# Kernel optimization log

Hardware: AMD Instinct MI355X
Metric: run time of the kernel (lower is better)

## Reference

```python
import jax, jax.numpy as jnp
import numpy as np

NUM_HEADS = 16
R_MIN = 16
R_MAX = 64


def setup_inputs() -> dict:
    key = jax.random.key(0)
    ks = jax.random.split(key, 12)
    bs, S, H = 4, 2048, 1024
    hidden_states = jax.random.normal(ks[0], (bs, S, H), dtype=jnp.float32)
    # Linear layers: y = x @ W.T + b (torch convention, W is [out, in])
    wscale = 1.0 / np.sqrt(H)
    Wq = jax.random.normal(ks[1], (H, H), dtype=jnp.float32) * wscale
    bq = jnp.zeros((H,), dtype=jnp.float32)
    Wk = jax.random.normal(ks[2], (H, H), dtype=jnp.float32) * wscale
    bk = jnp.zeros((H,), dtype=jnp.float32)
    Wv = jax.random.normal(ks[3], (H, H), dtype=jnp.float32) * wscale
    bv = jnp.zeros((H,), dtype=jnp.float32)
    Wo = jax.random.normal(ks[4], (H, H), dtype=jnp.float32) * wscale
    bo = jnp.zeros((H,), dtype=jnp.float32)
    # xavier_uniform for proj_k/proj_v over last two dims (seq_len, r_max)
    xs = float(np.sqrt(6.0 / (S + R_MAX)))
    proj_k = jax.random.uniform(ks[5], (NUM_HEADS, S, R_MAX), dtype=jnp.float32, minval=-xs, maxval=xs)
    proj_v = jax.random.uniform(ks[6], (NUM_HEADS, S, R_MAX), dtype=jnp.float32, minval=-xs, maxval=xs)
    return {
        'hidden_states': hidden_states,
        'Wq': Wq, 'bq': bq, 'Wk': Wk, 'bk': bk, 'Wv': Wv, 'bv': bv,
        'Wo': Wo, 'bo': bo, 'proj_k': proj_k, 'proj_v': proj_v,
    }


def reference(hidden_states, Wq, bq, Wk, bk, Wv, bv, Wo, bo, proj_k, proj_v):
    bs, S, H = hidden_states.shape
    nh = NUM_HEADS
    hd = H // nh

    def heads(x):  # [b,s,H] -> [b,h,s,d]
        return x.reshape(bs, S, nh, hd).transpose(0, 2, 1, 3)

    q = heads(hidden_states @ Wq.T + bq)
    k = heads(hidden_states @ Wk.T + bk)
    v = heads(hidden_states @ Wv.T + bv)

    # dynamic rank from per-sample variance (torch .var is unbiased -> ddof=1)
    batch_var = jnp.var(hidden_states.reshape(bs, -1), axis=1, ddof=1)
    var_norm = (batch_var - batch_var.min()) / (batch_var.max() - batch_var.min() + 1e-6)
    curr_r = jnp.round(R_MIN + var_norm.mean() * (R_MAX - R_MIN)).astype(jnp.int32)

    # low-rank projection of K/V along sequence; compute full r_max, mask at softmax
    key_proj = jnp.einsum('bhld,hlk->bhkd', k, proj_k)      # [b,h,R,d]
    value_proj = jnp.einsum('bhld,hlk->bhkd', v, proj_v)    # [b,h,R,d]

    scores = jnp.einsum('bhsd,bhkd->bhsk', q, key_proj) / jnp.sqrt(jnp.float32(hd))
    rank_mask = jnp.arange(R_MAX) < curr_r                  # [R]
    scores = jnp.where(rank_mask, scores, -jnp.inf)
    attn_probs = jax.nn.softmax(scores, axis=-1)            # zeros beyond curr_r
    # dropout is identity in eval mode
    context = jnp.einsum('bhsk,bhkd->bhsd', attn_probs, value_proj)
    context = context.transpose(0, 2, 1, 3).reshape(bs, S, H)
    output = context @ Wo.T + bo
    return output, attn_probs, curr_r
```

## Files before the change

kernel.cpp:

```cpp
#include <hip/hip_runtime.h>


typedef unsigned short u16;
typedef short s16x8 __attribute__((ext_vector_type(8)));
typedef unsigned short u16x8 __attribute__((ext_vector_type(8)));
typedef float f32x4 __attribute__((ext_vector_type(4)));

#define GLL16(gp, lp) __builtin_amdgcn_global_load_lds( \
    (const __attribute__((address_space(1))) void*)(gp), \
    (__attribute__((address_space(3))) void*)(lp), 16, 0, 0)

__device__ __forceinline__ u16 f2bf(float f) {
    unsigned u = __float_as_uint(f);
    u += 0x7fffu + ((u >> 16) & 1u);
    return (u16)(u >> 16);
}

__device__ __forceinline__ f32x4 mfma16(s16x8 a, s16x8 b, f32x4 c) {
    return __builtin_amdgcn_mfma_f32_16x16x32_bf16(a, b, c, 0, 0, 0);
}

__global__ __launch_bounds__(256) void cast_hs_var_k(const float* __restrict__ hs,
        u16* __restrict__ out, double* __restrict__ red) {
    int t = threadIdx.x;
    size_t base = (size_t)blockIdx.x * 8192;
    double s = 0.0, s2 = 0.0;
    #pragma unroll
    for (int i = 0; i < 4; ++i) {
        size_t idx = base + (size_t)i * 2048 + (size_t)t * 8;
        float4 a = *(const float4*)(hs + idx);
        float4 c = *(const float4*)(hs + idx + 4);
        s  += (double)a.x + (double)a.y + (double)a.z + (double)a.w
            + (double)c.x + (double)c.y + (double)c.z + (double)c.w;
        s2 += (double)a.x * a.x + (double)a.y * a.y + (double)a.z * a.z + (double)a.w * a.w
            + (double)c.x * c.x + (double)c.y * c.y + (double)c.z * c.z + (double)c.w * c.w;
        u16x8 o;
        o[0] = f2bf(a.x); o[1] = f2bf(a.y); o[2] = f2bf(a.z); o[3] = f2bf(a.w);
        o[4] = f2bf(c.x); o[5] = f2bf(c.y); o[6] = f2bf(c.z); o[7] = f2bf(c.w);
        *(u16x8*)(out + idx) = o;
    }
    __shared__ double sa[256], sb[256];
    sa[t] = s; sb[t] = s2;
    __syncthreads();
    for (int o = 128; o > 0; o >>= 1) {
        if (t < o) { sa[t] += sa[t + o]; sb[t] += sb[t + o]; }
        __syncthreads();
    }
    if (t == 0) { red[blockIdx.x * 2] = sa[0]; red[blockIdx.x * 2 + 1] = sb[0]; }
}

__global__ __launch_bounds__(256) void compute_r_k(const double* __restrict__ red,
        int* __restrict__ currp, float* __restrict__ outr) {
    int t = threadIdx.x, lane = t & 63, b = t >> 6;
    double s = 0.0, s2 = 0.0;
    #pragma unroll
    for (int j = 0; j < 4; ++j) {
        int idx = b * 256 + j * 64 + lane;
        s += red[idx * 2]; s2 += red[idx * 2 + 1];
    }
    #pragma unroll
    for (int o = 1; o < 64; o <<= 1) { s += __shfl_xor(s, o); s2 += __shfl_xor(s2, o); }
    __shared__ double vs[4];
    if (lane == 0) {
        const double N = 2097152.0;
        vs[b] = (s2 - s * s / N) / (N - 1.0);
    }
    __syncthreads();
    if (t == 0) {
        double mn = vs[0], mx = vs[0];
        for (int i = 1; i < 4; ++i) { mn = fmin(mn, vs[i]); mx = fmax(mx, vs[i]); }
        double mean = 0.0;
        for (int i = 0; i < 4; ++i) mean += (vs[i] - mn) / (mx - mn + 1e-6);
        mean *= 0.25;
        double r = rint(16.0 + mean * 48.0);
        *currp = (int)r;
        *outr = (float)r;
    }
}

__global__ __launch_bounds__(256) void prep_k(const float* __restrict__ w0,
        const float* __restrict__ w1, const float* __restrict__ w2,
        const float* __restrict__ w3, u16* __restrict__ wout,
        const float* __restrict__ p0, const float* __restrict__ p1,
        u16* __restrict__ q0, u16* __restrict__ q1,
        const float* __restrict__ bq, const float* __restrict__ bk,
        const float* __restrict__ bv, float* __restrict__ biascat) {
    __shared__ float tl[64][65];
    int bid = blockIdx.x, t = threadIdx.x;
    if (bid < 2048) {
        int mat = bid >> 9;
        int off = ((bid & 511) * 256 + t) * 8;
        const float* src = (mat == 0) ? w0 : (mat == 1) ? w1 : (mat == 2) ? w2 : w3;
        float4 a = *(const float4*)(src + off);
        float4 c = *(const float4*)(src + off + 4);
        u16x8 o;
        o[0] = f2bf(a.x); o[1] = f2bf(a.y); o[2] = f2bf(a.z); o[3] = f2bf(a.w);
        o[4] = f2bf(c.x); o[5] = f2bf(c.y); o[6] = f2bf(c.z); o[7] = f2bf(c.w);
        *(u16x8*)(wout + (size_t)mat * 1048576 + off) = o;
    } else if (bid < 3072) {
        int bid2 = bid - 2048;
        int which = bid2 >> 9, bi = bid2 & 511;
        const float* p = which ? p1 : p0;
        u16* pt = which ? q1 : q0;
        int h = bi >> 5, lb = bi & 31;
        {
            int l = t >> 2, r0 = (t & 3) * 16;
            const float* src = p + ((size_t)(h * 2048 + lb * 64 + l)) * 64 + r0;
            #pragma unroll
            for (int u = 0; u < 4; ++u) {
                float4 v = *(const float4*)(src + u * 4);
                tl[l][r0 + u * 4 + 0] = v.x; tl[l][r0 + u * 4 + 1] = v.y;
                tl[l][r0 + u * 4 + 2] = v.z; tl[l][r0 + u * 4 + 3] = v.w;
            }
        }
        __syncthreads();
        {
            int r = t >> 2, l0 = (t & 3) * 16;
            u16x8 o0, o1;
            #pragma unroll
            for (int j = 0; j < 8; ++j) { o0[j] = f2bf(tl[l0 + j][r]); o1[j] = f2bf(tl[l0 + 8 + j][r]); }
            u16* dst = pt + ((size_t)(h * 64 + r)) * 2048 + lb * 64 + l0;
            *(u16x8*)dst = o0;
            *(u16x8*)(dst + 8) = o1;
        }
    } else {
        for (int i = t; i < 3072; i += 256) {
            float v = (i < 1024) ? bq[i] : (i < 2048) ? bk[i - 1024] : bv[i - 2048];
            biascat[i] = v;
        }
    }
}

__global__ __launch_bounds__(512, 2) void qkv_gemm_k(const u16* __restrict__ Ag,
        const u16* __restrict__ Wcat, const float* __restrict__ biascat,
        u16* __restrict__ C) {
    __shared__ u16 lds[40960];
    int bid = blockIdx.x;
    int swz = (bid & 7) * 32 + (bid >> 3);
    int bm = swz >> 3, bn = swz & 7;
    int t = threadIdx.x, lane = t & 63, w = t >> 6, wr = w >> 2, wc = w & 3;

    int srow = w * 16 + (lane >> 2);
    int slog = (((lane & 3) ^ ((lane >> 3) & 3)) << 3);
    const u16* asrc0 = Ag + (size_t)(bm * 256 + srow) * 1024 + slog;
    const u16* bsrc0 = Wcat + (size_t)(bn * 384 + srow) * 1024 + slog;

#define STAGEA(kts, h) GLL16(asrc0 + (h) * 131072 + (kts) * 32, \
                             &lds[(((kts) & 1) * 8192) + (h) * 4096 + w * 512])
#define STAGEB(kts, h) GLL16(bsrc0 + (h) * 131072 + (kts) * 32, \
                             &lds[16384 + (((kts) & 1) * 12288) + (h) * 4096 + w * 512])

    int pcol = (((lane >> 4) ^ (((lane & 15) >> 1) & 3)) << 3);
    int arow0 = (wr * 128 + (lane & 15)) * 32 + pcol;
    int brow0 = 16384 + (wc * 96 + (lane & 15)) * 32 + pcol;

    f32x4 zero4 = {0.f, 0.f, 0.f, 0.f};
    f32x4 acc[8][6];
    #pragma unroll
    for (int m = 0; m < 8; ++m)
        #pragma unroll
        for (int n = 0; n < 6; ++n) acc[m][n] = zero4;

    STAGEA(0, 0); STAGEA(0, 1); STAGEB(0, 0); STAGEB(0, 1); STAGEB(0, 2);
    STAGEA(1, 0); STAGEA(1, 1);
    asm volatile("s_waitcnt vmcnt(2)" ::: "memory");
    __builtin_amdgcn_s_barrier();
    asm volatile("" ::: "memory");

    for (int kt = 0; kt < 32; ++kt) {
        int abase = (kt & 1) * 8192 + arow0;
        int bbase = (kt & 1) * 12288 + brow0;
        s16x8 af[8], bf0, bf1;

        #pragma unroll
        for (int m = 0; m < 8; ++m) af[m] = *(const s16x8*)&lds[abase + m * 512];
        bf0 = *(const s16x8*)&lds[bbase];
        bf1 = *(const s16x8*)&lds[bbase + 512];
        if (kt < 31) { STAGEB(kt + 1, 0); STAGEB(kt + 1, 1); }
        asm volatile("s_waitcnt lgkmcnt(0)" ::: "memory");
        __builtin_amdgcn_s_barrier();
        __builtin_amdgcn_s_setprio(1);
        #pragma unroll
        for (int m = 0; m < 8; ++m) {
            acc[m][0] = mfma16(af[m], bf0, acc[m][0]);
            acc[m][1] = mfma16(af[m], bf1, acc[m][1]);
        }
        __builtin_amdgcn_s_setprio(0);
        __builtin_amdgcn_s_barrier();
        asm volatile("" ::: "memory");

        bf0 = *(const s16x8*)&lds[bbase + 1024];
        bf1 = *(const s16x8*)&lds[bbase + 1536];
        if (kt < 31) STAGEB(kt + 1, 2);
        if (kt < 30) STAGEA(kt + 2, 0);
        asm volatile("s_waitcnt lgkmcnt(0)" ::: "memory");
        __builtin_amdgcn_s_barrier();
        __builtin_amdgcn_s_setprio(1);
        #pragma unroll
        for (int m = 0; m < 8; ++m) {
            acc[m][2] = mfma16(af[m], bf0, acc[m][2]);
            acc[m][3] = mfma16(af[m], bf1, acc[m][3]);
        }
        __builtin_amdgcn_s_setprio(0);
        __builtin_amdgcn_s_barrier();
        asm volatile("" ::: "memory");

        bf0 = *(const s16x8*)&lds[bbase + 2048];
        bf1 = *(const s16x8*)&lds[bbase + 2560];
        if (kt < 30) STAGEA(kt + 2, 1);
        if (kt < 30) { asm volatile("s_waitcnt vmcnt(2)" ::: "memory"); }
        else if (kt == 30) { asm volatile("s_waitcnt vmcnt(0)" ::: "memory"); }
        asm volatile("s_waitcnt lgkmcnt(0)" ::: "memory");
        __builtin_amdgcn_s_barrier();
        __builtin_amdgcn_s_setprio(1);
        #pragma unroll
        for (int m = 0; m < 8; ++m) {
            acc[m][4] = mfma16(af[m], bf0, acc[m][4]);
            acc[m][5] = mfma16(af[m], bf1, acc[m][5]);
        }
        __builtin_amdgcn_s_setprio(0);
        __builtin_amdgcn_s_barrier();
        asm volatile("" ::: "memory");
    }

    float bias[6];
    #pragma unroll
    for (int n = 0; n < 6; ++n)
        bias[n] = biascat[bn * 384 + wc * 96 + n * 16 + (lane & 15)];
    #pragma unroll
    for (int m = 0; m < 8; ++m) {
        int row0 = bm * 256 + wr * 128 + m * 16 + ((lane >> 4) << 2);
        #pragma unroll
        for (int n = 0; n < 6; ++n) {
            int col = bn * 384 + wc * 96 + n * 16 + (lane & 15);
            #pragma unroll
            for (int v = 0; v < 4; ++v)
                C[(size_t)(row0 + v) * 3072 + col] = f2bf(acc[m][n][v] + bias[n]);
        }
    }
#undef STAGEA
#undef STAGEB
}

__global__ __launch_bounds__(256) void gemm_bt_k(const u16* __restrict__ Ag,
        const u16* __restrict__ Bg, const float* __restrict__ biasg,
        float* __restrict__ Cg) {
    __shared__ u16 at[2][4096];
    __shared__ u16 bt[2][4096];
    int bm = blockIdx.x, bn = blockIdx.y;
    int t = threadIdx.x, lane = t & 63, w = t >> 6, wr = w >> 1, wc = w & 1;
    const u16* ag = Ag + (size_t)(bm * 128 + w * 32 + (lane >> 2)) * 1024 + (lane & 3) * 8;
    const u16* bg = Bg + (size_t)(bn * 128 + w * 32 + (lane >> 2)) * 1024 + (lane & 3) * 8;

    f32x4 zero4 = {0.f, 0.f, 0.f, 0.f};
    f32x4 acc[4][4];
    #pragma unroll
    for (int i = 0; i < 4; ++i)
        #pragma unroll
        for (int j = 0; j < 4; ++j) acc[i][j] = zero4;

    GLL16(ag,         &at[0][w * 1024]);
    GLL16(ag + 16384, &at[0][w * 1024 + 512]);
    GLL16(bg,         &bt[0][w * 1024]);
    GLL16(bg + 16384, &bt[0][w * 1024 + 512]);
    __syncthreads();

    int cur = 0;
    for (int kk = 0; kk < 32; ++kk) {
        if (kk < 31) {
            const u16* an = ag + (kk + 1) * 32;
            const u16* bn2 = bg + (kk + 1) * 32;
            GLL16(an,          &at[cur ^ 1][w * 1024]);
            GLL16(an + 16384,  &at[cur ^ 1][w * 1024 + 512]);
            GLL16(bn2,         &bt[cur ^ 1][w * 1024]);
            GLL16(bn2 + 16384, &bt[cur ^ 1][w * 1024 + 512]);
        }
        s16x8 af[4], bf[4];
        #pragma unroll
        for (int i = 0; i < 4; ++i)
            af[i] = *(const s16x8*)&at[cur][(wr * 64 + i * 16 + (lane & 15)) * 32 + (lane >> 4) * 8];
        #pragma unroll
        for (int j = 0; j < 4; ++j)
            bf[j] = *(const s16x8*)&bt[cur][(wc * 64 + j * 16 + (lane & 15)) * 32 + (lane >> 4) * 8];
        #pragma unroll
        for (int i = 0; i < 4; ++i)
            #pragma unroll
            for (int j = 0; j < 4; ++j) acc[i][j] = mfma16(af[i], bf[j], acc[i][j]);
        __syncthreads();
        cur ^= 1;
    }

    #pragma unroll
    for (int i = 0; i < 4; ++i) {
        int row0 = bm * 128 + wr * 64 + i * 16 + ((lane >> 4) << 2);
        #pragma unroll
        for (int j = 0; j < 4; ++j) {
            int col = bn * 128 + wc * 64 + j * 16 + (lane & 15);
            float bias = biasg[col];
            #pragma unroll
            for (int v = 0; v < 4; ++v)
                Cg[(size_t)(row0 + v) * 1024 + col] = acc[i][j][v] + bias;
        }
    }
}

__global__ __launch_bounds__(256) void proj_einsum_k(const u16* __restrict__ qkv,
        const u16* __restrict__ pt0, const u16* __restrict__ pt1,
        float* __restrict__ out0, float* __restrict__ out1) {
    __shared__ u16 kt[256 * 66];
    int c = blockIdx.x, h = blockIdx.y, z = blockIdx.z;
    int which = z >> 2, b = z & 3;
    const u16* kv = qkv + 1024 + which * 1024;
    const u16* pt = which ? pt1 : pt0;
    float* outp = which ? out1 : out0;
    int t = threadIdx.x, lane = t & 63, w = t >> 6;

    int tl = t >> 3, sd = (t & 7) * 8;
    const u16* kvp = kv + (size_t)(b * 2048 + c * 256 + tl) * 3072 + h * 64 + sd;
    s16x8 g[8];
    #pragma unroll
    for (int i = 0; i < 8; ++i) g[i] = *(const s16x8*)(kvp + (size_t)i * 98304);
    #pragma unroll
    for (int i = 0; i < 8; ++i) *(s16x8*)&kt[(tl + 32 * i) * 66 + sd] = g[i];
    __syncthreads();

    f32x4 zero4 = {0.f, 0.f, 0.f, 0.f};
    f32x4 acc[4] = {zero4, zero4, zero4, zero4};
    const u16* ptb_ = pt + (size_t)(h * 64 + (lane & 15)) * 2048 + c * 256 + ((lane >> 4) << 3);
    int gcol = w * 16 + (lane & 15);
    int gk0 = (lane >> 4) << 3;

    #pragma unroll
    for (int ks = 0; ks < 8; ++ks) {
        s16x8 bf;
        int kb = (ks * 32 + gk0) * 66 + gcol;
        #pragma unroll
        for (int j = 0; j < 8; ++j) bf[j] = (short)kt[kb + j * 66];
        #pragma unroll
        for (int m = 0; m < 4; ++m) {
            s16x8 af = *(const s16x8*)(ptb_ + (size_t)m * 32768 + ks * 32);
            acc[m] = mfma16(af, bf, acc[m]);
        }
    }

    float* ob = outp + (size_t)((c * 4 + b) * 16 + h) * 4096;
    #pragma unroll
    for (int m = 0; m < 4; ++m)
        #pragma unroll
        for (int v = 0; v < 4; ++v)
            ob[(m * 16 + ((lane >> 4) << 2) + v) * 64 + w * 16 + (lane & 15)] = acc[m][v];
}

__global__ __launch_bounds__(256) void reduce_kv_k(const float* __restrict__ kp_part,
        const float* __restrict__ vp_part, u16* __restrict__ kpb, u16* __restrict__ vpb) {
    int h = blockIdx.x, b = blockIdx.y, t = threadIdx.x;
    int base = (b * 16 + h) * 4096 + t * 16;
    float4 zf = {0.f, 0.f, 0.f, 0.f};
    float4 sk[4] = {zf, zf, zf, zf}, sv[4] = {zf, zf, zf, zf};
    #pragma unroll
    for (int c = 0; c < 8; ++c) {
        #pragma unroll
        for (int u = 0; u < 4; ++u) {
            float4 a = *(const float4*)&kp_part[c * 262144 + base + u * 4];
            float4 g = *(const float4*)&vp_part[c * 262144 + base + u * 4];
            sk[u].x += a.x; sk[u].y += a.y; sk[u].z += a.z; sk[u].w += a.w;
            sv[u].x += g.x; sv[u].y += g.y; sv[u].z += g.z; sv[u].w += g.w;
        }
    }
    int r = t >> 2, d0 = (t & 3) * 16;
    size_t ob = (size_t)(b * 16 + h) * 4096;
    u16x8 o0, o1;
    o0[0] = f2bf(sk[0].x); o0[1] = f2bf(sk[0].y); o0[2] = f2bf(sk[0].z); o0[3] = f2bf(sk[0].w);
    o0[4] = f2bf(sk[1].x); o0[5] = f2bf(sk[1].y); o0[6] = f2bf(sk[1].z); o0[7] = f2bf(sk[1].w);
    o1[0] = f2bf(sk[2].x); o1[1] = f2bf(sk[2].y); o1[2] = f2bf(sk[2].z); o1[3] = f2bf(sk[2].w);
    o1[4] = f2bf(sk[3].x); o1[5] = f2bf(sk[3].y); o1[6] = f2bf(sk[3].z); o1[7] = f2bf(sk[3].w);
    *(u16x8*)&kpb[ob + r * 64 + d0]     = o0;
    *(u16x8*)&kpb[ob + r * 64 + d0 + 8] = o1;
    #pragma unroll
    for (int u = 0; u < 4; ++u) {
        int d = d0 + u * 4;
        vpb[ob + (size_t)(d + 0) * 64 + r] = f2bf(sv[u].x);
        vpb[ob + (size_t)(d + 1) * 64 + r] = f2bf(sv[u].y);
        vpb[ob + (size_t)(d + 2) * 64 + r] = f2bf(sv[u].z);
        vpb[ob + (size_t)(d + 3) * 64 + r] = f2bf(sv[u].w);
    }
}

__global__ __launch_bounds__(256) void attn_k(const u16* __restrict__ qkv,
        const u16* __restrict__ kpb, const u16* __restrict__ vpb,
        const int* __restrict__ currp, float* __restrict__ probs, u16* __restrict__ ctxb) {
    int sb = blockIdx.x, h = blockIdx.y, b = blockIdx.z;
    int cr = *currp;
    __shared__ u16 kpl[64 * 80];
    __shared__ u16 vpl[64 * 80];
    __shared__ u16 pl[64 * 80];
    int t = threadIdx.x, lane = t & 63, w = t >> 6;

    {
        int r = t >> 2, d0 = (t & 3) * 16;
        size_t ob = (size_t)(b * 16 + h) * 4096 + t * 16;
        u16x8 k0 = *(const u16x8*)(kpb + ob), k1 = *(const u16x8*)(kpb + ob + 8);
        u16x8 v0 = *(const u16x8*)(vpb + ob), v1 = *(const u16x8*)(vpb + ob + 8);
        *(u16x8*)&kpl[r * 80 + d0]     = k0;
        *(u16x8*)&kpl[r * 80 + d0 + 8] = k1;
        *(u16x8*)&vpl[r * 80 + d0]     = v0;
        *(u16x8*)&vpl[r * 80 + d0 + 8] = v1;
    }
    __syncthreads();

    const u16* qp = qkv + (size_t)(b * 2048 + sb * 64 + w * 16 + (lane & 15)) * 3072 + h * 64 + ((lane >> 4) << 3);
    s16x8 q0 = *(const s16x8*)qp;
    s16x8 q1 = *(const s16x8*)(qp + 32);
    f32x4 zero4 = {0.f, 0.f, 0.f, 0.f};
    f32x4 sc[4];
    #pragma unroll
    for (int j = 0; j < 4; ++j) {
        sc[j] = zero4;
        s16x8 k0 = *(const s16x8*)&kpl[(j * 16 + (lane & 15)) * 80 + ((lane >> 4) << 3)];
        s16x8 k1 = *(const s16x8*)&kpl[(j * 16 + (lane & 15)) * 80 + 32 + ((lane >> 4) << 3)];
        sc[j] = mfma16(q0, k0, sc[j]);
        sc[j] = mfma16(q1, k1, sc[j]);
    }

    const float scale = 0.125f;
    float p_[4][4];
    #pragma unroll
    for (int v = 0; v < 4; ++v) {
        float m = -3.0e38f;
        #pragma unroll
        for (int j = 0; j < 4; ++j) {
            int rr = j * 16 + (lane & 15);
            if (rr < cr) m = fmaxf(m, sc[j][v] * scale);
        }
        m = fmaxf(m, __shfl_xor(m, 1));
        m = fmaxf(m, __shfl_xor(m, 2));
        m = fmaxf(m, __shfl_xor(m, 4));
        m = fmaxf(m, __shfl_xor(m, 8));
        float s = 0.f;
        #pragma unroll
        for (int j = 0; j < 4; ++j) {
            int rr = j * 16 + (lane & 15);
            float p = (rr < cr) ? __expf(sc[j][v] * scale - m) : 0.f;
            p_[j][v] = p; s += p;
        }
        s += __shfl_xor(s, 1); s += __shfl_xor(s, 2);
        s += __shfl_xor(s, 4); s += __shfl_xor(s, 8);
        float inv = 1.f / s;
        #pragma unroll
        for (int j = 0; j < 4; ++j) p_[j][v] *= inv;
    }

    int srow = w * 16 + ((lane >> 4) << 2);
    #pragma unroll
    for (int v = 0; v < 4; ++v) {
        int sg = sb * 64 + srow + v;
        #pragma unroll
        for (int j = 0; j < 4; ++j) {
            int rr = j * 16 + (lane & 15);
            probs[(size_t)((b * 16 + h) * 2048 + sg) * 64 + rr] = p_[j][v];
            pl[(srow + v) * 80 + rr] = f2bf(p_[j][v]);
        }
    }
    __syncthreads();

    f32x4 co[4] = {zero4, zero4, zero4, zero4};
    #pragma unroll
    for (int ks = 0; ks < 2; ++ks) {
        s16x8 pa = *(const s16x8*)&pl[(w * 16 + (lane & 15)) * 80 + ks * 32 + ((lane >> 4) << 3)];
        #pragma unroll
        for (int n = 0; n < 4; ++n) {
            s16x8 vf = *(const s16x8*)&vpl[(n * 16 + (lane & 15)) * 80 + ks * 32 + ((lane >> 4) << 3)];
            co[n] = mfma16(pa, vf, co[n]);
        }
    }
    #pragma unroll
    for (int n = 0; n < 4; ++n)
        #pragma unroll
        for (int v = 0; v < 4; ++v)
            ctxb[(size_t)((b * 2048 + sb * 64 + srow + v) * 16 + h) * 64 + n * 16 + (lane & 15)] = f2bf(co[n][v]);
}

extern "C" void kernel_launch(void* const* d_in, const int* in_sizes, int n_in,
                              void* d_out, int out_size, void* d_ws, size_t ws_size,
                              hipStream_t stream) {
    const float* hs = (const float*)d_in[0];
    const float* Wq = (const float*)d_in[1];
    const float* bq = (const float*)d_in[2];
    const float* Wk = (const float*)d_in[3];
    const float* bk = (const float*)d_in[4];
    const float* Wv = (const float*)d_in[5];
    const float* bv = (const float*)d_in[6];
    const float* Wo = (const float*)d_in[7];
    const float* bo = (const float*)d_in[8];
    const float* pk = (const float*)d_in[9];
    const float* pv = (const float*)d_in[10];
    float* out = (float*)d_out;
    char* w = (char*)d_ws;

    u16* hsb   = (u16*)(w + 0);
    float* vp_part = (float*)(w + 0);
    u16* ctxb  = (u16*)(w + 0);
    u16* wqb   = (u16*)(w + 16777216);
    u16* ptb   = (u16*)(w + 25165824);
    u16* pvtb  = (u16*)(w + 29360128);
    u16* qkvb  = (u16*)(w + 33554432);
    float* kp_part = (float*)(w + 83886080);
    float* biascat = (float*)(w + 92274688);
    double* red    = (double*)(w + 92291072);
    int* currp     = (int*)(w + 92307456);
    u16* kpb   = (u16*)(w + 92307520);
    u16* vpb   = (u16*)(w + 92831808);

    cast_hs_var_k<<<1024, 256, 0, stream>>>(hs, hsb, red);
    compute_r_k<<<1, 256, 0, stream>>>(red, currp, out + 16777216);
    prep_k<<<3073, 256, 0, stream>>>(Wq, Wk, Wv, Wo, wqb, pk, pv, ptb, pvtb,
                                     bq, bk, bv, biascat);

    qkv_gemm_k<<<256, 512, 0, stream>>>(hsb, wqb, biascat, qkvb);

    proj_einsum_k<<<dim3(8, 16, 8), 256, 0, stream>>>(qkvb, ptb, pvtb, kp_part, vp_part);
    reduce_kv_k<<<dim3(16, 4), 256, 0, stream>>>(kp_part, vp_part, kpb, vpb);

    attn_k<<<dim3(32, 16, 4), 256, 0, stream>>>(qkvb, kpb, vpb, currp,
                                                out + 8388608, ctxb);

    gemm_bt_k<<<dim3(64, 8), 256, 0, stream>>>(ctxb, wqb + 3145728, bo, out);
}
```

Before: 154.8 us.

## Rewrite output projection GEMM with larger tiles, swizzled LDS, and phased pipeline

The output projection GEMM becomes a 512-thread kernel with 256x128 tiles, XOR-swizzled LDS staging via global_load_lds, a block-index swizzle for L2 locality, and the same two-phase prefetch/barrier schedule the QKV GEMM uses. The QKV GEMM inner loop also drops from three MFMA phases to two per k-step, with three B fragments per phase, which cuts barriers. The aim is less LDS bank conflict and synchronisation overhead and better operand reuse. The cost is higher register pressure and fewer blocks (256) to fill the GPU.

```diff
diff --git a/kernel.cpp b/kernel.cpp
--- a/kernel.cpp
+++ b/kernel.cpp
@@ -170,13 +170,14 @@
     for (int kt = 0; kt < 32; ++kt) {
         int abase = (kt & 1) * 8192 + arow0;
         int bbase = (kt & 1) * 12288 + brow0;
-        s16x8 af[8], bf0, bf1;
+        s16x8 af[8], bf0, bf1, bf2;
 
         #pragma unroll
         for (int m = 0; m < 8; ++m) af[m] = *(const s16x8*)&lds[abase + m * 512];
         bf0 = *(const s16x8*)&lds[bbase];
         bf1 = *(const s16x8*)&lds[bbase + 512];
-        if (kt < 31) { STAGEB(kt + 1, 0); STAGEB(kt + 1, 1); }
+        bf2 = *(const s16x8*)&lds[bbase + 1024];
+        if (kt < 31) { STAGEB(kt + 1, 0); STAGEB(kt + 1, 1); STAGEB(kt + 1, 2); }
         asm volatile("s_waitcnt lgkmcnt(0)" ::: "memory");
         __builtin_amdgcn_s_barrier();
         __builtin_amdgcn_s_setprio(1);
@@ -184,30 +185,16 @@
         for (int m = 0; m < 8; ++m) {
             acc[m][0] = mfma16(af[m], bf0, acc[m][0]);
             acc[m][1] = mfma16(af[m], bf1, acc[m][1]);
+            acc[m][2] = mfma16(af[m], bf2, acc[m][2]);
         }
         __builtin_amdgcn_s_setprio(0);
         __builtin_amdgcn_s_barrier();
         asm volatile("" ::: "memory");
 
-        bf0 = *(const s16x8*)&lds[bbase + 1024];
-        bf1 = *(const s16x8*)&lds[bbase + 1536];
-        if (kt < 31) STAGEB(kt + 1, 2);
-        if (kt < 30) STAGEA(kt + 2, 0);
-        asm volatile("s_waitcnt lgkmcnt(0)" ::: "memory");
-        __builtin_amdgcn_s_barrier();
-        __builtin_amdgcn_s_setprio(1);
-        #pragma unroll
-        for (int m = 0; m < 8; ++m) {
-            acc[m][2] = mfma16(af[m], bf0, acc[m][2]);
-            acc[m][3] = mfma16(af[m], bf1, acc[m][3]);
-        }
-        __builtin_amdgcn_s_setprio(0);
-        __builtin_amdgcn_s_barrier();
-        asm volatile("" ::: "memory");
-
-        bf0 = *(const s16x8*)&lds[bbase + 2048];
-        bf1 = *(const s16x8*)&lds[bbase + 2560];
-        if (kt < 30) STAGEA(kt + 2, 1);
+        bf0 = *(const s16x8*)&lds[bbase + 1536];
+        bf1 = *(const s16x8*)&lds[bbase + 2048];
+        bf2 = *(const s16x8*)&lds[bbase + 2560];
+        if (kt < 30) { STAGEA(kt + 2, 0); STAGEA(kt + 2, 1); }
         if (kt < 30) { asm volatile("s_waitcnt vmcnt(2)" ::: "memory"); }
         else if (kt == 30) { asm volatile("s_waitcnt vmcnt(0)" ::: "memory"); }
         asm volatile("s_waitcnt lgkmcnt(0)" ::: "memory");
@@ -215,8 +202,9 @@
         __builtin_amdgcn_s_setprio(1);
         #pragma unroll
         for (int m = 0; m < 8; ++m) {
-            acc[m][4] = mfma16(af[m], bf0, acc[m][4]);
-            acc[m][5] = mfma16(af[m], bf1, acc[m][5]);
+            acc[m][3] = mfma16(af[m], bf0, acc[m][3]);
+            acc[m][4] = mfma16(af[m], bf1, acc[m][4]);
+            acc[m][5] = mfma16(af[m], bf2, acc[m][5]);
         }
         __builtin_amdgcn_s_setprio(0);
         __builtin_amdgcn_s_barrier();
@@ -242,66 +230,99 @@
 #undef STAGEB
 }
 
-__global__ __launch_bounds__(256) void gemm_bt_k(const u16* __restrict__ Ag,
+__global__ __launch_bounds__(512, 2) void out_gemm_k(const u16* __restrict__ Ag,
         const u16* __restrict__ Bg, const float* __restrict__ biasg,
         float* __restrict__ Cg) {
-    __shared__ u16 at[2][4096];
-    __shared__ u16 bt[2][4096];
-    int bm = blockIdx.x, bn = blockIdx.y;
+    __shared__ u16 lds[24576];
+    int bid = blockIdx.x;
+    int swz = (bid & 7) * 32 + (bid >> 3);
+    int bm = swz >> 3, bn = swz & 7;
     int t = threadIdx.x, lane = t & 63, w = t >> 6, wr = w >> 1, wc = w & 1;
-    const u16* ag = Ag + (size_t)(bm * 128 + w * 32 + (lane >> 2)) * 1024 + (lane & 3) * 8;
-    const u16* bg = Bg + (size_t)(bn * 128 + w * 32 + (lane >> 2)) * 1024 + (lane & 3) * 8;
+
+    int srow = w * 16 + (lane >> 2);
+    int slog = (((lane & 3) ^ ((lane >> 3) & 3)) << 3);
+    const u16* asrc0 = Ag + (size_t)(bm * 256 + srow) * 1024 + slog;
+    const u16* bsrc0 = Bg + (size_t)(bn * 128 + srow) * 1024 + slog;
+
+#define STAGEA(kts, h) GLL16(asrc0 + (h) * 131072 + (kts) * 32, \
+                             &lds[(((kts) & 1) * 8192) + (h) * 4096 + w * 512])
+#define STAGEB(kts) GLL16(bsrc0 + (kts) * 32, \
+                          &lds[16384 + (((kts) & 1) * 4096) + w * 512])
+
+    int pcol = (((lane >> 4) ^ (((lane & 15) >> 1) & 3)) << 3);
+    int arow0 = (wr * 64 + (lane & 15)) * 32 + pcol;
+    int brow0 = 16384 + (wc * 64 + (lane & 15)) * 32 + pcol;
 
     f32x4 zero4 = {0.f, 0.f, 0.f, 0.f};
     f32x4 acc[4][4];
     #pragma unroll
-    for (int i = 0; i < 4; ++i)
-        #pragma unroll
-        for (int j = 0; j < 4; ++j) acc[i][j] = zero4;
-
-    GLL16(ag,         &at[0][w * 1024]);
-    GLL16(ag + 16384, &at[0][w * 1024 + 512]);
-    GLL16(bg,         &bt[0][w * 1024]);
-    GLL16(bg + 16384, &bt[0][w * 1024 + 512]);
-    __syncthreads();
-
-    int cur = 0;
-    for (int kk = 0; kk < 32; ++kk) {
-        if (kk < 31) {
-            const u16* an = ag + (kk + 1) * 32;
-            const u16* bn2 = bg + (kk + 1) * 32;
-            GLL16(an,          &at[cur ^ 1][w * 1024]);
-            GLL16(an + 16384,  &at[cur ^ 1][w * 1024 + 512]);
-            GLL16(bn2,         &bt[cur ^ 1][w * 1024]);
-            GLL16(bn2 + 16384, &bt[cur ^ 1][w * 1024 + 512]);
-        }
-        s16x8 af[4], bf[4];
-        #pragma unroll
-        for (int i = 0; i < 4; ++i)
-            af[i] = *(const s16x8*)&at[cur][(wr * 64 + i * 16 + (lane & 15)) * 32 + (lane >> 4) * 8];
-        #pragma unroll
-        for (int j = 0; j < 4; ++j)
-            bf[j] = *(const s16x8*)&bt[cur][(wc * 64 + j * 16 + (lane & 15)) * 32 + (lane >> 4) * 8];
-        #pragma unroll
-        for (int i = 0; i < 4; ++i)
-            #pragma unroll
-            for (int j = 0; j < 4; ++j) acc[i][j] = mfma16(af[i], bf[j], acc[i][j]);
-        __syncthreads();
-        cur ^= 1;
-    }
-
-    #pragma unroll
-    for (int i = 0; i < 4; ++i) {
-        int row0 = bm * 128 + wr * 64 + i * 16 + ((lane >> 4) << 2);
-        #pragma unroll
-        for (int j = 0; j < 4; ++j) {
-            int col = bn * 128 + wc * 64 + j * 16 + (lane & 15);
-            float bias = biasg[col];
+    for (int m = 0; m < 4; ++m)
+        #pragma unroll
+        for (int n = 0; n < 4; ++n) acc[m][n] = zero4;
+
+    STAGEA(0, 0); STAGEA(0, 1); STAGEB(0);
+    STAGEA(1, 0); STAGEA(1, 1);
+    asm volatile("s_waitcnt vmcnt(2)" ::: "memory");
+    __builtin_amdgcn_s_barrier();
+    asm volatile("" ::: "memory");
+
+    for (int kt = 0; kt < 32; ++kt) {
+        int abase = (kt & 1) * 8192 + arow0;
+        int bbase = (kt & 1) * 4096 + brow0;
+        s16x8 af[4], bf0, bf1;
+
+        #pragma unroll
+        for (int m = 0; m < 4; ++m) af[m] = *(const s16x8*)&lds[abase + m * 512];
+        bf0 = *(const s16x8*)&lds[bbase];
+        bf1 = *(const s16x8*)&lds[bbase + 512];
+        if (kt < 31) STAGEB(kt + 1);
+        asm volatile("s_waitcnt lgkmcnt(0)" ::: "memory");
+        __builtin_amdgcn_s_barrier();
+        __builtin_amdgcn_s_setprio(1);
+        #pragma unroll
+        for (int m = 0; m < 4; ++m) {
+            acc[m][0] = mfma16(af[m], bf0, acc[m][0]);
+            acc[m][1] = mfma16(af[m], bf1, acc[m][1]);
+        }
+        __builtin_amdgcn_s_setprio(0);
+        __builtin_amdgcn_s_barrier();
+        asm volatile("" ::: "memory");
+
+        bf0 = *(const s16x8*)&lds[bbase + 1024];
+        bf1 = *(const s16x8*)&lds[bbase + 1536];
+        if (kt < 30) { STAGEA(kt + 2, 0); STAGEA(kt + 2, 1); }
+        if (kt < 30) { asm volatile("s_waitcnt vmcnt(2)" ::: "memory"); }
+        else if (kt == 30) { asm volatile("s_waitcnt vmcnt(0)" ::: "memory"); }
+        asm volatile("s_waitcnt lgkmcnt(0)" ::: "memory");
+        __builtin_amdgcn_s_barrier();
+        __builtin_amdgcn_s_setprio(1);
+        #pragma unroll
+        for (int m = 0; m < 4; ++m) {
+            acc[m][2] = mfma16(af[m], bf0, acc[m][2]);
+            acc[m][3] = mfma16(af[m], bf1, acc[m][3]);
+        }
+        __builtin_amdgcn_s_setprio(0);
+        __builtin_amdgcn_s_barrier();
+        asm volatile("" ::: "memory");
+    }
+
+    float bias[4];
+    #pragma unroll
+    for (int n = 0; n < 4; ++n)
+        bias[n] = biasg[bn * 128 + wc * 64 + n * 16 + (lane & 15)];
+    #pragma unroll
+    for (int m = 0; m < 4; ++m) {
+        int row0 = bm * 256 + wr * 64 + m * 16 + ((lane >> 4) << 2);
+        #pragma unroll
+        for (int n = 0; n < 4; ++n) {
+            int col = bn * 128 + wc * 64 + n * 16 + (lane & 15);
             #pragma unroll
             for (int v = 0; v < 4; ++v)
-                Cg[(size_t)(row0 + v) * 1024 + col] = acc[i][j][v] + bias;
-        }
-    }
+                Cg[(size_t)(row0 + v) * 1024 + col] = acc[m][n][v] + bias[n];
+        }
+    }
+#undef STAGEA
+#undef STAGEB
 }
 
 __global__ __launch_bounds__(256) void proj_einsum_k(const u16* __restrict__ qkv,
@@ -524,5 +545,5 @@
     attn_k<<<dim3(32, 16, 4), 256, 0, stream>>>(qkvb, kpb, vpb, currp,
                                                 out + 8388608, ctxb);
 
-    gemm_bt_k<<<dim3(64, 8), 256, 0, stream>>>(ctxb, wqb + 3145728, bo, out);
-}
+    out_gemm_k<<<256, 512, 0, stream>>>(ctxb, wqb + 3145728, bo, out);
+}
```

Result: no change. 154.8 us (+0.0%).
